# Kernel tuning notes

Hardware: AMD Instinct MI355X
Metric: run time of the kernel (lower is better)

The kernel has to match this reference:

```python
import jax, jax.numpy as jnp
import numpy as np

B, FR, D = 32, 300, 2048
E, G, K = 2, 8, 64
FEAT = E * D // G          # 512
VLAD = K * FEAT            # 32768
H, R = 2048, 8
NC = 3862
BN_EPS = 1e-5
L2_EPS = 1e-12


def _bn(x, g, b, m, v):
    # eval-mode BatchNorm1d with running stats
    return (x - m) * jax.lax.rsqrt(v + BN_EPS) * g + b


def _l2n(x, axis):
    # torch F.normalize: x / max(||x||, eps)
    n = jnp.sqrt(jnp.sum(x * x, axis=axis, keepdims=True))
    return x / jnp.maximum(n, L2_EPS)


def setup_inputs() -> dict:
    key = jax.random.key(0)
    ks = jax.random.split(key, 10)
    rn = lambda k, s: jax.random.normal(k, s, jnp.float32) * 0.02
    return {
        "x": jax.random.normal(ks[0], (B, FR, D), jnp.float32),
        "fc1_w": rn(ks[1], (E * D, D)), "fc1_b": jnp.zeros((E * D,), jnp.float32),
        "fc2_w": rn(ks[2], (G, E * D)), "fc2_b": jnp.zeros((G,), jnp.float32),
        "c1": jax.random.uniform(ks[3], (E * D, G * K), jnp.float32),
        "c2": jax.random.uniform(ks[4], (1, FEAT, K), jnp.float32),
        "bn1_g": jnp.ones((G * K,), jnp.float32), "bn1_b": jnp.zeros((G * K,), jnp.float32),
        "bn1_m": jnp.zeros((G * K,), jnp.float32), "bn1_v": jnp.ones((G * K,), jnp.float32),
        "bn2_g": jnp.ones((VLAD,), jnp.float32), "bn2_b": jnp.zeros((VLAD,), jnp.float32),
        "bn2_m": jnp.zeros((VLAD,), jnp.float32), "bn2_v": jnp.ones((VLAD,), jnp.float32),
        "cgf_w": rn(ks[5], (H, VLAD)), "cgf_b": jnp.zeros((H,), jnp.float32),
        "cgbn_g": jnp.ones((H,), jnp.float32), "cgbn_b": jnp.zeros((H,), jnp.float32),
        "cgbn_m": jnp.zeros((H,), jnp.float32), "cgbn_v": jnp.ones((H,), jnp.float32),
        "g1_w": rn(ks[6], (H // R, H)), "g1_b": jnp.zeros((H // R,), jnp.float32),
        "gbn_g": jnp.ones((H // R,), jnp.float32), "gbn_b": jnp.zeros((H // R,), jnp.float32),
        "gbn_m": jnp.zeros((H // R,), jnp.float32), "gbn_v": jnp.ones((H // R,), jnp.float32),
        "g2_w": rn(ks[7], (H, H // R)), "g2_b": jnp.zeros((H,), jnp.float32),
        "fc3_w": rn(ks[8], (NC, H)), "fc3_b": jnp.zeros((NC,), jnp.float32),
    }


def _forward(x, fc1_w, fc1_b, fc2_w, fc2_b, c1, c2,
             bn1_g, bn1_b, bn1_m, bn1_v, bn2_g, bn2_b, bn2_m, bn2_v,
             cgf_w, cgf_b, cgbn_g, cgbn_b, cgbn_m, cgbn_v,
             g1_w, g1_b, gbn_g, gbn_b, gbn_m, gbn_v, g2_w, g2_b, fc3_w, fc3_b):
    b, fr, d = x.shape
    xn = _l2n(x, 2)                                      # per-frame L2 normalize
    h = xn @ fc1_w.T + fc1_b                             # [B,FR,E*D]
    att = jax.nn.sigmoid(h @ fc2_w.T + fc2_b)            # [B,FR,G]
    att = att.reshape(b, fr * G, 1)
    act = jnp.einsum('bfd,dc->bfc', h, c1)               # [B,FR,G*K]
    act = _bn(act, bn1_g, bn1_b, bn1_m, bn1_v)
    act = act.reshape(b, fr * G, K)
    act = jax.nn.softmax(act, axis=-1) * att             # soft-assign * attention
    a = act.sum(axis=1, keepdims=True) * c2              # [B,FEAT,K] via broadcast
    res = h.reshape(b, fr * G, FEAT)
    vlad = jnp.einsum('bnk,bnf->bfk', act, res) - a      # [B,FEAT,K]
    vlad = _l2n(vlad, 1).reshape(b, VLAD)                # intra-norm, flatten feat-major
    vlad = _bn(vlad, bn2_g, bn2_b, bn2_m, bn2_v)
    # SE context gating (dropout identity in reference)
    y = _bn(vlad @ cgf_w.T + cgf_b, cgbn_g, cgbn_b, cgbn_m, cgbn_v)   # [B,H]
    gate = jax.nn.sigmoid(
        jax.nn.relu(_bn(y @ g1_w.T + g1_b, gbn_g, gbn_b, gbn_m, gbn_v)) @ g2_w.T + g2_b)
    return (y * gate) @ fc3_w.T + fc3_b                  # [B,NC]


def reference(x, fc1_w, fc1_b, fc2_w, fc2_b, c1, c2,
              bn1_g, bn1_b, bn1_m, bn1_v, bn2_g, bn2_b, bn2_m, bn2_v,
              cgf_w, cgf_b, cgbn_g, cgbn_b, cgbn_m, cgbn_v,
              g1_w, g1_b, gbn_g, gbn_b, gbn_m, gbn_v, g2_w, g2_b, fc3_w, fc3_b):
    return _forward(x, fc1_w, fc1_b, fc2_w, fc2_b, c1, c2,
                    bn1_g, bn1_b, bn1_m, bn1_v, bn2_g, bn2_b, bn2_m, bn2_v,
                    cgf_w, cgf_b, cgbn_g, cgbn_b, cgbn_m, cgbn_v,
                    g1_w, g1_b, gbn_g, gbn_b, gbn_m, gbn_v, g2_w, g2_b, fc3_w, fc3_b)
```

## Files before the change

### kernel.cpp

```cpp
#include <hip/hip_runtime.h>

typedef unsigned short u16;
typedef unsigned int u32;
using f32x4 = __attribute__((ext_vector_type(4))) float;
using s16x8 = __attribute__((ext_vector_type(8))) short;
using u16x4 = __attribute__((ext_vector_type(4))) u16;

#define DEV __device__ __forceinline__

DEV float bf2f(u16 u) { union { u32 i; float f; } v; v.i = ((u32)u) << 16; return v.f; }
DEV u16 f2bf(float f) {
  union { float ff; u32 uu; } v; v.ff = f;
  u32 r = (v.uu + 0x7fffu + ((v.uu >> 16) & 1u)) >> 16;
  return (u16)r;
}

DEV void gl_lds16(const void* g, void* l) {
  __builtin_amdgcn_global_load_lds(
      (const __attribute__((address_space(1))) u32*)g,
      (__attribute__((address_space(3))) u32*)l, 16, 0, 0);
}

DEV void BAR() { __builtin_amdgcn_s_barrier(); }
DEV void VM6() { asm volatile("s_waitcnt vmcnt(6)" ::: "memory"); }
DEV void VM0() { asm volatile("s_waitcnt vmcnt(0)" ::: "memory"); }
DEV void PRIO1() { __builtin_amdgcn_s_setprio(1); }
DEV void PRIO0() { __builtin_amdgcn_s_setprio(0); }
#define LGKM0S() do { asm volatile("s_waitcnt lgkmcnt(0)" ::: "memory"); \
                      __builtin_amdgcn_sched_barrier(0); } while (0)

#define DSR(d, a, OFF) asm volatile("ds_read_b128 %0, %1 offset:" #OFF \
                                    : "=&v"(d) : "v"(a))
#define READ12(A_, B_, aa, bb) do {                                            \
  unsigned a_ = (aa), b_ = (bb);                                               \
  DSR(A_[0], a_, 0);     DSR(A_[1], a_, 2048);                                 \
  DSR(A_[2], a_, 4096);  DSR(A_[3], a_, 6144);                                 \
  DSR(A_[4], a_, 8192);  DSR(A_[5], a_, 10240);                                \
  DSR(A_[6], a_, 12288); DSR(A_[7], a_, 14336);                                \
  DSR(B_[0], b_, 0);     DSR(B_[1], b_, 2048);                                 \
  DSR(B_[2], b_, 4096);  DSR(B_[3], b_, 6144);                                 \
} while (0)

#define MFMA32(A_, B_) do {                                                    \
  _Pragma("unroll")                                                            \
  for (int i_ = 0; i_ < 8; i_++) {                                             \
    acc[i_][0] = __builtin_amdgcn_mfma_f32_16x16x32_bf16(A_[i_], B_[0], acc[i_][0], 0, 0, 0); \
    acc[i_][1] = __builtin_amdgcn_mfma_f32_16x16x32_bf16(A_[i_], B_[1], acc[i_][1], 0, 0, 0); \
    acc[i_][2] = __builtin_amdgcn_mfma_f32_16x16x32_bf16(A_[i_], B_[2], acc[i_][2], 0, 0, 0); \
    acc[i_][3] = __builtin_amdgcn_mfma_f32_16x16x32_bf16(A_[i_], B_[3], acc[i_][3], 0, 0, 0); \
  }                                                                            \
} while (0)

__global__ __launch_bounds__(256) void k_l2norm(const float* __restrict__ x, u16* __restrict__ xn) {
  int r = blockIdx.x, t = threadIdx.x;
  const float* xr = x + (size_t)r * 2048;
  float v[8], s = 0.f;
#pragma unroll
  for (int i = 0; i < 8; i++) { v[i] = xr[t + i*256]; s += v[i]*v[i]; }
#pragma unroll
  for (int off = 32; off > 0; off >>= 1) s += __shfl_xor(s, off, 64);
  __shared__ float red[4];
  if ((t & 63) == 0) red[t >> 6] = s;
  __syncthreads();
  float inv = 1.f / fmaxf(sqrtf(red[0]+red[1]+red[2]+red[3]), 1e-12f);
  u16* xo = xn + (size_t)r * 2048;
#pragma unroll
  for (int i = 0; i < 8; i++) xo[t + i*256] = f2bf(v[i]*inv);
}

__global__ void k_cvt(const float* __restrict__ in, u16* __restrict__ out, int n4) {
  int i = blockIdx.x*256 + threadIdx.x, st = gridDim.x*256;
  for (; i < n4; i += st) {
    f32x4 v = ((const f32x4*)in)[i];
    u16x4 o;
    o[0] = f2bf(v[0]); o[1] = f2bf(v[1]); o[2] = f2bf(v[2]); o[3] = f2bf(v[3]);
    ((u16x4*)out)[i] = o;
  }
}

__global__ __launch_bounds__(256) void k_transpose(const float* __restrict__ c1, u16* __restrict__ c1t) {
  __shared__ float tile[32][33];
  int k0 = blockIdx.x*32, n0 = blockIdx.y*32;
  int tx = threadIdx.x & 31, ty = threadIdx.x >> 5;
  for (int i = ty; i < 32; i += 8) tile[i][tx] = c1[(size_t)(k0+i)*512 + n0 + tx];
  __syncthreads();
  for (int i = ty; i < 32; i += 8) c1t[(size_t)(n0+i)*4096 + k0 + tx] = f2bf(tile[tx][i]);
}

template<bool WF32, bool WBF16>
__global__ __launch_bounds__(256) void k_gemm(
    const u16* __restrict__ A, const u16* __restrict__ Bt, const float* __restrict__ bias,
    float* __restrict__ Cf, u16* __restrict__ Cb, int N, int K, int Nlim,
    int MT, int NT, int swz) {
  __shared__ u16 As[128*32];
  __shared__ u16 Bs[128*32];
  int bid = blockIdx.x, mt, nt;
  if (swz) {
    int mg = (MT + 7) >> 3;
    int gid = bid >> 5, gl = bid & 31;
    mt = (gid % mg)*8 + (gl & 7);
    nt = (gid / mg)*4 + (gl >> 3);
    if (mt >= MT) return;
  } else { mt = bid % MT; nt = bid / MT; }
  int t = threadIdx.x, wv = t >> 6;
  int quad = (t & 63) >> 4, lr = t & 15;
  size_t m0 = (size_t)mt * 128, n0 = (size_t)nt * 128;
  int wm = wv & 1, wn = wv >> 1;
  int srow = t >> 2;
  int scol = (((t & 3) ^ ((t >> 3) & 3)) * 8);
  const u16* gA = A + (m0 + srow)*(size_t)K + scol;
  const u16* gB = Bt + (n0 + srow)*(size_t)K + scol;
  u16* lA = &As[wv*512];
  u16* lB = &Bs[wv*512];
  int xq = (quad ^ ((lr >> 1) & 3)) * 8;
  f32x4 acc[4][4];
#pragma unroll
  for (int i = 0; i < 4; i++)
#pragma unroll
    for (int j = 0; j < 4; j++) acc[i][j] = (f32x4){0.f,0.f,0.f,0.f};
  for (int k0 = 0; k0 < K; k0 += 32) {
    gl_lds16(gA + k0, lA);
    gl_lds16(gA + (size_t)64*K + k0, lA + 2048);
    gl_lds16(gB + k0, lB);
    gl_lds16(gB + (size_t)64*K + k0, lB + 2048);
    __syncthreads();
    s16x8 af[4], bfr[4];
#pragma unroll
    for (int i = 0; i < 4; i++) {
      af[i]  = *(const s16x8*)&As[(wm*64 + i*16 + lr)*32 + xq];
      bfr[i] = *(const s16x8*)&Bs[(wn*64 + i*16 + lr)*32 + xq];
    }
#pragma unroll
    for (int i = 0; i < 4; i++)
#pragma unroll
      for (int j = 0; j < 4; j++)
        acc[i][j] = __builtin_amdgcn_mfma_f32_16x16x32_bf16(af[i], bfr[j], acc[i][j], 0, 0, 0);
    __syncthreads();
  }
#pragma unroll
  for (int j = 0; j < 4; j++) {
    size_t nn = n0 + wn*64 + j*16 + lr;
    if ((int)nn >= Nlim) continue;
    float bj = bias ? bias[nn] : 0.f;
#pragma unroll
    for (int i = 0; i < 4; i++) {
      size_t mr = m0 + wm*64 + i*16 + quad*4;
#pragma unroll
      for (int r = 0; r < 4; r++) {
        float v = acc[i][j][r] + bj;
        if (WF32)  Cf[(mr + r)*N + nn] = v;
        if (WBF16) Cb[(mr + r)*N + nn] = f2bf(v);
      }
    }
  }
}

template<bool WF32, bool WBF16>
__global__ __launch_bounds__(512, 2) void k_gemm256(
    const u16* __restrict__ A, const u16* __restrict__ Bt, const float* __restrict__ bias,
    float* __restrict__ Cf, u16* __restrict__ Cb,
    int M, int N, int K, int Nlim, int MT, int NT, int swz) {
  constexpr int TILE = 256*64;
  __shared__ u16 lds[4*TILE];
  int bid = blockIdx.x, mt, nt;
  if (swz == 2) {
    int x = bid & 7, w2 = bid >> 3;
    mt = (x & 1)*19 + w2 % 19;
    nt = (x >> 1)*4 + w2 / 19;
  } else if (swz == 1) {
    int c = (MT*NT) >> 3; int b2 = (bid & 7)*c + (bid >> 3);
    mt = b2 % MT; nt = b2 / MT;
  } else { mt = bid % MT; nt = bid / MT; }
  int t = threadIdx.x, wv = t >> 6, lane = t & 63;
  int quad = lane >> 4, lr = lane & 15;
  int wm = wv >> 2, wn = wv & 3;
  size_t m0 = (size_t)mt * 256, n0 = (size_t)nt * 256;
  int srow = wv*8 + (lane >> 3);
  int schunk = ((lane & 7) ^ (lane >> 3)) * 8;
  const u16* gA = A  + (size_t)(m0 + srow)*K + schunk;
  const u16* gB = Bt + (size_t)(n0 + srow)*K + schunk;
  size_t row64 = (size_t)64 * K;
  int lofs = wv*512;
  unsigned ldsB = (unsigned)(size_t)lds;
  unsigned pc = (unsigned)((quad ^ (lr & 7)) << 4);
  unsigned aCur = ldsB + (unsigned)((wm*128 + lr)*128) + pc;
  unsigned bCur = ldsB + 32768u + (unsigned)((wn*64 + lr)*128) + pc;
  f32x4 acc[8][4];
#pragma unroll
  for (int i = 0; i < 8; i++)
#pragma unroll
    for (int j = 0; j < 4; j++) acc[i][j] = (f32x4){0.f,0.f,0.f,0.f};

  int T = K >> 6;
  u16* A0 = lds;            u16* B0 = lds + TILE;
  u16* A1 = lds + 2*TILE;   u16* B1 = lds + 3*TILE;
#pragma unroll
  for (int q = 0; q < 4; q++) gl_lds16(gA + q*row64, A0 + q*4096 + lofs);
#pragma unroll
  for (int q = 0; q < 4; q++) gl_lds16(gB + q*row64, B0 + q*4096 + lofs);
#pragma unroll
  for (int q = 0; q < 4; q++) gl_lds16(gA + 64 + q*row64, A1 + q*4096 + lofs);
  gl_lds16(gB + 64,          B1 + lofs);
  gl_lds16(gB + 64 + row64,  B1 + 4096 + lofs);
  VM6();
  BAR();

  s16x8 fa[8], fb[4];
  for (int tt = 0; tt < T; ++tt) {
    READ12(fa, fb, aCur, bCur);
    if (tt + 1 < T) {
      const u16* gB1 = gB + (size_t)(tt + 1)*64;
      u16* Bq = lds + (((tt + 1) & 1)*2 + 1)*TILE;
      gl_lds16(gB1 + 2*row64, Bq + 2*4096 + lofs);
      gl_lds16(gB1 + 3*row64, Bq + 3*4096 + lofs);
    }
    LGKM0S();
    PRIO1(); MFMA32(fa, fb); PRIO0();
    BAR();
    READ12(fa, fb, aCur ^ 64u, bCur ^ 64u);
    LGKM0S();
    PRIO1(); MFMA32(fa, fb); PRIO0();
    BAR();
    if (tt + 2 < T) {
      const u16* gA2 = gA + (size_t)(tt + 2)*64;
      const u16* gB2 = gB + (size_t)(tt + 2)*64;
      u16* Ap = lds + ((tt & 1)*2)*TILE;
      u16* Bp = Ap + TILE;
#pragma unroll
      for (int q = 0; q < 4; q++) gl_lds16(gA2 + q*row64, Ap + q*4096 + lofs);
      gl_lds16(gB2,         Bp + lofs);
      gl_lds16(gB2 + row64, Bp + 4096 + lofs);
      VM6();
    } else if (tt + 1 < T) {
      VM0();
    }
    if (tt + 1 < T) BAR();
    aCur ^= 0x10000u; bCur ^= 0x10000u;
  }

  float bj[4];
#pragma unroll
  for (int j = 0; j < 4; j++) {
    int nn = (int)n0 + wn*64 + j*16 + lr;
    bj[j] = (bias && nn < Nlim) ? bias[nn] : 0.f;
  }
#pragma unroll
  for (int i = 0; i < 8; i++) {
    int mrb = (int)m0 + wm*128 + i*16 + quad*4;
#pragma unroll
    for (int r = 0; r < 4; r++) {
      int mr = mrb + r;
      if (mr >= M) continue;
#pragma unroll
      for (int j = 0; j < 4; j++) {
        int nn = (int)n0 + wn*64 + j*16 + lr;
        if (nn >= Nlim) continue;
        float v = acc[i][j][r] + bj[j];
        if (WF32)  Cf[(size_t)mr*N + nn] = v;
        if (WBF16) Cb[(size_t)mr*N + nn] = f2bf(v);
      }
    }
  }
}

__global__ __launch_bounds__(256) void k_hbt(const u16* __restrict__ hb, u16* __restrict__ hbT) {
  __shared__ u16 tile[64*33];
  int nt = blockIdx.x, ft = blockIdx.y, b = blockIdx.z, t = threadIdx.x;
  int n0 = nt*32, f0 = ft*64;
  int rrel = t >> 6, g = (t >> 3) & 7, fi = (t & 7)*8;
  const u16* src = hb + ((size_t)(b*300 + (n0 >> 3) + rrel))*4096 + g*512 + f0 + fi;
  u16 v[8];
  *(u16x4*)v = *(const u16x4*)src;
  *(u16x4*)(v+4) = *(const u16x4*)(src+4);
  int nl = rrel*8 + g;
#pragma unroll
  for (int e = 0; e < 8; e++) tile[(fi+e)*33 + nl] = v[e];
  __syncthreads();
  int f = t >> 2, nc = (t & 3)*8;
  u16 o[8];
#pragma unroll
  for (int e = 0; e < 8; e++) o[e] = tile[f*33 + nc + e];
  u16* dst = hbT + ((size_t)b*512 + f0 + f)*2400 + n0 + nc;
  *(u16x4*)dst = *(u16x4*)o;
  *(u16x4*)(dst+4) = *(u16x4*)(o+4);
}

__global__ __launch_bounds__(512) void k_softmax(const float* __restrict__ act_ext,
    const float* __restrict__ fc2_b,
    const float* __restrict__ g, const float* __restrict__ b,
    const float* __restrict__ mu, const float* __restrict__ var, u16* __restrict__ actT) {
  int m = blockIdx.x, t = threadIdx.x;
  int bb = m / 300, fr = m - bb*300;
  int gi = t >> 6, k = t & 63, c = t;
  float v = act_ext[(size_t)m*640 + c];
  v = (v - mu[c]) * rsqrtf(var[c] + 1e-5f) * g[c] + b[c];
  float mx = v;
#pragma unroll
  for (int off = 32; off > 0; off >>= 1) mx = fmaxf(mx, __shfl_xor(mx, off, 64));
  float e = __expf(v - mx);
  float s = e;
#pragma unroll
  for (int off = 32; off > 0; off >>= 1) s += __shfl_xor(s, off, 64);
  float attl = act_ext[(size_t)m*640 + 512 + gi] + fc2_b[gi];
  float attv = 1.f / (1.f + __expf(-attl));
  float r = (e / s) * attv;
  __shared__ u16 st[64*9];
  st[k*9 + gi] = f2bf(r);
  __syncthreads();
  if (t < 64) {
    u16 o[8];
#pragma unroll
    for (int e2 = 0; e2 < 8; e2++) o[e2] = st[t*9 + e2];
    u16* dst = actT + ((size_t)bb*64 + t)*2400 + fr*8;
    *(u16x4*)dst = *(u16x4*)o;
    *(u16x4*)(dst+4) = *(u16x4*)(o+4);
  }
}

__global__ __launch_bounds__(256) void k_asum(const u16* __restrict__ actT, float* __restrict__ a_sum) {
  int b = blockIdx.x, t = threadIdx.x;
  int k = t >> 2, q = t & 3;
  const u16* p = actT + ((size_t)b*64 + k)*2400 + q*600;
  float acc = 0.f;
  for (int j = 0; j < 600; j += 8) {
    u16x4 a0 = *(const u16x4*)(p + j);
    u16x4 a1 = *(const u16x4*)(p + j + 4);
    acc += bf2f(a0[0])+bf2f(a0[1])+bf2f(a0[2])+bf2f(a0[3])
         + bf2f(a1[0])+bf2f(a1[1])+bf2f(a1[2])+bf2f(a1[3]);
  }
  __shared__ float red[256];
  red[t] = acc;
  __syncthreads();
  if (t < 64) a_sum[b*64 + t] = red[t*4] + red[t*4+1] + red[t*4+2] + red[t*4+3];
}

__global__ __launch_bounds__(256) void k_vlad(const u16* __restrict__ hbT, const u16* __restrict__ actT,
                                              float* __restrict__ P2) {
  __shared__ u16 As[128*32];
  __shared__ u16 Bs[64*32];
  int t = threadIdx.x, wv = t >> 6;
  int quad = (t & 63) >> 4, lr = t & 15;
  int ft = blockIdx.x, b = blockIdx.y, ns = blockIdx.z;
  int wm = wv & 1, wn = wv >> 1;
  int srow = t >> 2;
  int scol = (((t & 3) ^ ((t >> 3) & 3)) * 8);
  int xq = (quad ^ ((lr >> 1) & 3)) * 8;
  const u16* gA = hbT + ((size_t)b*512 + ft*128 + srow)*2400 + ns*480 + scol;
  const u16* gB = actT + ((size_t)b*64 + srow)*2400 + ns*480 + scol;
  u16* lA = &As[wv*512];
  u16* lB = &Bs[wv*512];
  f32x4 acc[4][2];
#pragma unroll
  for (int i = 0; i < 4; i++)
#pragma unroll
    for (int j = 0; j < 2; j++) acc[i][j] = (f32x4){0.f,0.f,0.f,0.f};
  for (int k0 = 0; k0 < 480; k0 += 32) {
    gl_lds16(gA + k0, lA);
    gl_lds16(gA + (size_t)64*2400 + k0, lA + 2048);
    gl_lds16(gB + k0, lB);
    __syncthreads();
    s16x8 af[4], bfr[2];
#pragma unroll
    for (int i = 0; i < 4; i++)
      af[i] = *(const s16x8*)&As[(wm*64 + i*16 + lr)*32 + xq];
#pragma unroll
    for (int j = 0; j < 2; j++)
      bfr[j] = *(const s16x8*)&Bs[(wn*32 + j*16 + lr)*32 + xq];
#pragma unroll
    for (int i = 0; i < 4; i++)
#pragma unroll
      for (int j = 0; j < 2; j++)
        acc[i][j] = __builtin_amdgcn_mfma_f32_16x16x32_bf16(af[i], bfr[j], acc[i][j], 0, 0, 0);
    __syncthreads();
  }
  size_t base = ((size_t)ns*32 + b)*512*64;
#pragma unroll
  for (int j = 0; j < 2; j++) {
    int kc = wn*32 + j*16 + lr;
#pragma unroll
    for (int i = 0; i < 4; i++) {
      int f = ft*128 + wm*64 + i*16 + quad*4;
#pragma unroll
      for (int r = 0; r < 4; r++)
        P2[base + (size_t)(f + r)*64 + kc] = acc[i][j][r];
    }
  }
}

__global__ __launch_bounds__(256) void k_norm2(const float* __restrict__ P2, const float* __restrict__ a_sum,
    const float* __restrict__ c2, const float* __restrict__ g, const float* __restrict__ b,
    const float* __restrict__ mu, const float* __restrict__ var, float* __restrict__ out) {
  int k = blockIdx.x, bb = blockIdx.y, t = threadIdx.x;
  float as = a_sum[bb*64 + k];
  int f0 = t, f1 = t + 256;
  const size_t PS = (size_t)32*512*64;
  size_t base = (size_t)bb*512*64;
  float x0 = 0.f, x1 = 0.f;
#pragma unroll
  for (int ns = 0; ns < 5; ns++) {
    x0 += P2[ns*PS + base + (size_t)f0*64 + k];
    x1 += P2[ns*PS + base + (size_t)f1*64 + k];
  }
  x0 -= as * c2[f0*64 + k];
  x1 -= as * c2[f1*64 + k];
  float s = x0*x0 + x1*x1;
#pragma unroll
  for (int off = 32; off > 0; off >>= 1) s += __shfl_xor(s, off, 64);
  __shared__ float red[4];
  if ((t & 63) == 0) red[t >> 6] = s;
  __syncthreads();
  float inv = 1.f / fmaxf(sqrtf(red[0]+red[1]+red[2]+red[3]), 1e-12f);
  int c0 = f0*64 + k, c1 = f1*64 + k;
  out[(size_t)bb*32768 + c0] = (x0*inv - mu[c0]) * rsqrtf(var[c0]+1e-5f) * g[c0] + b[c0];
  out[(size_t)bb*32768 + c1] = (x1*inv - mu[c1]) * rsqrtf(var[c1]+1e-5f) * g[c1] + b[c1];
}

__global__ __launch_bounds__(256) void k_skgemm(
    const float* __restrict__ A, const float* __restrict__ W,
    float* __restrict__ P, int N, int K, int KC, int Npad) {
  constexpr int LDB = 72;
  __shared__ u16 Bs[128*LDB];
  __shared__ u16 As[32*LDB];
  int t = threadIdx.x;
  int wv = t >> 6, quad = (t & 63) >> 4, lr = t & 15;
  int n0 = blockIdx.x * 128;
  size_t kc0 = (size_t)blockIdx.y * KC;
  f32x4 acc[2][2];
#pragma unroll
  for (int i = 0; i < 2; i++)
#pragma unroll
    for (int j = 0; j < 2; j++) acc[i][j] = (f32x4){0.f,0.f,0.f,0.f};
  int wl[8]; size_t wg[8];
#pragma unroll
  for (int i = 0; i < 8; i++) {
    int slot = i*256 + t;
    int r = slot >> 4, q = slot & 15;
    int row = n0 + r; if (row >= N) row = N - 1;
    wl[i] = r*LDB + q*4;
    wg[i] = (size_t)row*K + kc0 + q*4;
  }
  int al[2]; size_t ag[2];
#pragma unroll
  for (int i = 0; i < 2; i++) {
    int slot = i*256 + t;
    int r = slot >> 4, q = slot & 15;
    al[i] = r*LDB + q*4;
    ag[i] = (size_t)r*K + kc0 + q*4;
  }
  int nst = KC >> 6;
  f32x4 wv4[8], av4[2];
#pragma unroll
  for (int i = 0; i < 8; i++) wv4[i] = *(const f32x4*)(W + wg[i]);
#pragma unroll
  for (int i = 0; i < 2; i++) av4[i] = *(const f32x4*)(A + ag[i]);
  for (int s = 0; s < nst; s++) {
    if (s) __syncthreads();
#pragma unroll
    for (int i = 0; i < 8; i++) {
      u16x4 o;
      o[0] = f2bf(wv4[i][0]); o[1] = f2bf(wv4[i][1]);
      o[2] = f2bf(wv4[i][2]); o[3] = f2bf(wv4[i][3]);
      *(u16x4*)&Bs[wl[i]] = o;
    }
#pragma unroll
    for (int i = 0; i < 2; i++) {
      u16x4 o;
      o[0] = f2bf(av4[i][0]); o[1] = f2bf(av4[i][1]);
      o[2] = f2bf(av4[i][2]); o[3] = f2bf(av4[i][3]);
      *(u16x4*)&As[al[i]] = o;
    }
    __syncthreads();
    if (s + 1 < nst) {
      int off = (s + 1) * 64;
#pragma unroll
      for (int i = 0; i < 8; i++) wv4[i] = *(const f32x4*)(W + wg[i] + off);
#pragma unroll
      for (int i = 0; i < 2; i++) av4[i] = *(const f32x4*)(A + ag[i] + off);
    }
#pragma unroll
    for (int ks = 0; ks < 2; ks++) {
      s16x8 af[2];
#pragma unroll
      for (int i = 0; i < 2; i++)
        af[i] = *(const s16x8*)&As[(i*16 + lr)*LDB + ks*32 + quad*8];
#pragma unroll
      for (int j = 0; j < 2; j++) {
        s16x8 bf = *(const s16x8*)&Bs[(wv*32 + j*16 + lr)*LDB + ks*32 + quad*8];
#pragma unroll
        for (int i = 0; i < 2; i++)
          acc[i][j] = __builtin_amdgcn_mfma_f32_16x16x32_bf16(af[i], bf, acc[i][j], 0, 0, 0);
      }
    }
  }
#pragma unroll
  for (int i = 0; i < 2; i++)
#pragma unroll
    for (int j = 0; j < 2; j++) {
      int n = n0 + wv*32 + j*16 + lr;
#pragma unroll
      for (int r = 0; r < 4; r++) {
        int m = i*16 + quad*4 + r;
        P[((size_t)blockIdx.y*32 + m)*Npad + n] = acc[i][j][r];
      }
    }
}

template<int EPI>
__global__ __launch_bounds__(256) void k_skred(const float* __restrict__ P, int KSPLIT, int N, int Npad,
    const float* __restrict__ bias, const float* __restrict__ bg, const float* __restrict__ bb,
    const float* __restrict__ bm, const float* __restrict__ bv, float* __restrict__ C) {
  int idx = blockIdx.x*256 + threadIdx.x;
  if (idx >= 32*N) return;
  int m = idx / N, n = idx - m*N;
  float s = 0.f;
  for (int k = 0; k < KSPLIT; k++) s += P[((size_t)k*32 + m)*Npad + n];
  float v = s + (bias ? bias[n] : 0.f);
  if (EPI == 1 || EPI == 2) {
    v = (v - bm[n]) * rsqrtf(bv[n] + 1e-5f) * bg[n] + bb[n];
    if (EPI == 2) v = fmaxf(v, 0.f);
  } else if (EPI == 3) {
    v = 1.f / (1.f + __expf(-v));
  }
  C[idx] = v;
}

__global__ void k_mul(const float* __restrict__ a, const float* __restrict__ b, float* __restrict__ o, int n) {
  int i = blockIdx.x*256 + threadIdx.x;
  if (i < n) o[i] = a[i]*b[i];
}

extern "C" void kernel_launch(void* const* d_in, const int* in_sizes, int n_in,
                              void* d_out, int out_size, void* d_ws, size_t ws_size,
                              hipStream_t stream) {
  (void)in_sizes; (void)n_in; (void)out_size; (void)ws_size;
  const float* x      = (const float*)d_in[0];
  const float* fc1_w  = (const float*)d_in[1];
  const float* fc1_b  = (const float*)d_in[2];
  const float* fc2_w  = (const float*)d_in[3];
  const float* fc2_b  = (const float*)d_in[4];
  const float* c1     = (const float*)d_in[5];
  const float* c2     = (const float*)d_in[6];
  const float* bn1_g  = (const float*)d_in[7];
  const float* bn1_b  = (const float*)d_in[8];
  const float* bn1_m  = (const float*)d_in[9];
  const float* bn1_v  = (const float*)d_in[10];
  const float* bn2_g  = (const float*)d_in[11];
  const float* bn2_b  = (const float*)d_in[12];
  const float* bn2_m  = (const float*)d_in[13];
  const float* bn2_v  = (const float*)d_in[14];
  const float* cgf_w  = (const float*)d_in[15];
  const float* cgf_b  = (const float*)d_in[16];
  const float* cgbn_g = (const float*)d_in[17];
  const float* cgbn_b = (const float*)d_in[18];
  const float* cgbn_m = (const float*)d_in[19];
  const float* cgbn_v = (const float*)d_in[20];
  const float* g1_w   = (const float*)d_in[21];
  const float* g1_b   = (const float*)d_in[22];
  const float* gbn_g  = (const float*)d_in[23];
  const float* gbn_b  = (const float*)d_in[24];
  const float* gbn_m  = (const float*)d_in[25];
  const float* gbn_v  = (const float*)d_in[26];
  const float* g2_w   = (const float*)d_in[27];
  const float* g2_b   = (const float*)d_in[28];
  const float* fc3_w  = (const float*)d_in[29];
  const float* fc3_b  = (const float*)d_in[30];

  char* w = (char*)d_ws;
  u16*   xn    = (u16*)  (w + 0);
  u16*   w1b   = (u16*)  (w + 39321600);
  u16*   hbT   = (u16*)  (w + 0);
  u16*   hb    = (u16*)  (w + 78643200);
  u16*   c1ext = (u16*)  (w + 157286400);
  float* actx  = (float*)(w + 162529280);
  u16*   actT  = (u16*)  (w + 187105280);
  float* P2    = (float*)(w + 196935680);
  float* P     = (float*)(w + 196935680);
  float* a_sum = (float*)(w + 217907200);
  float* vladn = (float*)(w + 217915392);
  float* y     = (float*)(w + 222109696);
  float* z     = (float*)(w + 222371840);
  float* gate  = (float*)(w + 222404608);
  float* yg    = (float*)(w + 222666752);

  k_l2norm<<<9600, 256, 0, stream>>>(x, xn);
  k_cvt<<<2048, 256, 0, stream>>>(fc1_w, w1b, (4096*2048)/4);
  k_transpose<<<dim3(128, 16), 256, 0, stream>>>(c1, c1ext);
  k_cvt<<<32, 256, 0, stream>>>(fc2_w, c1ext + (size_t)512*4096, (8*4096)/4);
  k_gemm256<false, true><<<608, 512, 0, stream>>>(xn, w1b, fc1_b, nullptr, hb,
                                                  9600, 4096, 2048, 4096, 38, 16, 2);
  k_hbt<<<dim3(75, 8, 32), 256, 0, stream>>>(hb, hbT);
  k_gemm<true, false><<<375, 256, 0, stream>>>(hb, c1ext, nullptr, actx, nullptr, 640, 4096, 520, 75, 5, 0);
  k_softmax<<<9600, 512, 0, stream>>>(actx, fc2_b, bn1_g, bn1_b, bn1_m, bn1_v, actT);
  k_asum<<<32, 256, 0, stream>>>(actT, a_sum);
  k_vlad<<<dim3(4, 32, 5), 256, 0, stream>>>(hbT, actT, P2);
  k_norm2<<<dim3(64, 32), 256, 0, stream>>>(P2, a_sum, c2, bn2_g, bn2_b, bn2_m, bn2_v, vladn);

  k_skgemm<<<dim3(16, 64), 256, 0, stream>>>(vladn, cgf_w, P, 2048, 32768, 512, 2048);
  k_skred<1><<<256, 256, 0, stream>>>(P, 64, 2048, 2048, cgf_b, cgbn_g, cgbn_b, cgbn_m, cgbn_v, y);
  k_skgemm<<<dim3(2, 32), 256, 0, stream>>>(y, g1_w, P, 256, 2048, 64, 256);
  k_skred<2><<<32, 256, 0, stream>>>(P, 32, 256, 256, g1_b, gbn_g, gbn_b, gbn_m, gbn_v, z);
  k_skgemm<<<dim3(16, 4), 256, 0, stream>>>(z, g2_w, P, 2048, 256, 64, 2048);
  k_skred<3><<<256, 256, 0, stream>>>(P, 4, 2048, 2048, g2_b, nullptr, nullptr, nullptr, nullptr, gate);
  k_mul<<<256, 256, 0, stream>>>(y, gate, yg, 65536);
  k_skgemm<<<dim3(31, 16), 256, 0, stream>>>(yg, fc3_w, P, 3862, 2048, 128, 3968);
  k_skred<0><<<483, 256, 0, stream>>>(P, 16, 3862, 3968, fc3_b, nullptr, nullptr, nullptr, nullptr, (float*)d_out);
}
```

Baseline: 1.003 ms.

## Software-pipeline LDS fragment reads with MFMA in GEMM main loop

The GEMM inner loop now reads LDS fragments in quarter-sized groups into double-buffered register sets. Partial lgkmcnt waits let each group of 16 MFMAs run while the next ds_reads are in flight, replacing the old read-all-then-wait-all pattern. One mid-iteration barrier is removed and the next tile's first fragments are prefetched across the loop boundary. This costs more VGPRs for the extra fragment buffers, which may lower occupancy, and depends on the lgkmcnt counts exactly matching the issue order of the reads.

New measurement: 992.0 us. About the same (-1.1%).

```diff
diff --git a/kernel.cpp b/kernel.cpp
--- a/kernel.cpp
+++ b/kernel.cpp
@@ -21,35 +21,29 @@
       (__attribute__((address_space(3))) u32*)l, 16, 0, 0);
 }
 
-DEV void BAR() { __builtin_amdgcn_s_barrier(); }
+DEV void BAR() { __builtin_amdgcn_s_barrier(); __builtin_amdgcn_sched_barrier(0); }
 DEV void VM6() { asm volatile("s_waitcnt vmcnt(6)" ::: "memory"); }
 DEV void VM0() { asm volatile("s_waitcnt vmcnt(0)" ::: "memory"); }
 DEV void PRIO1() { __builtin_amdgcn_s_setprio(1); }
 DEV void PRIO0() { __builtin_amdgcn_s_setprio(0); }
-#define LGKM0S() do { asm volatile("s_waitcnt lgkmcnt(0)" ::: "memory"); \
-                      __builtin_amdgcn_sched_barrier(0); } while (0)
+#define SBAR0() __builtin_amdgcn_sched_barrier(0)
+#define LGKM(N_) do { asm volatile("s_waitcnt lgkmcnt(" #N_ ")" ::: "memory"); SBAR0(); } while (0)
 
 #define DSR(d, a, OFF) asm volatile("ds_read_b128 %0, %1 offset:" #OFF \
                                     : "=&v"(d) : "v"(a))
-#define READ12(A_, B_, aa, bb) do {                                            \
-  unsigned a_ = (aa), b_ = (bb);                                               \
-  DSR(A_[0], a_, 0);     DSR(A_[1], a_, 2048);                                 \
-  DSR(A_[2], a_, 4096);  DSR(A_[3], a_, 6144);                                 \
-  DSR(A_[4], a_, 8192);  DSR(A_[5], a_, 10240);                                \
-  DSR(A_[6], a_, 12288); DSR(A_[7], a_, 14336);                                \
-  DSR(B_[0], b_, 0);     DSR(B_[1], b_, 2048);                                 \
-  DSR(B_[2], b_, 4096);  DSR(B_[3], b_, 6144);                                 \
-} while (0)
-
-#define MFMA32(A_, B_) do {                                                    \
+#define DSR4(D_, a_) do { unsigned aa_ = (a_);                                 \
+  DSR(D_[0], aa_, 0);    DSR(D_[1], aa_, 2048);                                \
+  DSR(D_[2], aa_, 4096); DSR(D_[3], aa_, 6144); } while (0)
+
+#define MF16(FA_, FB_, R_) do { PRIO1();                                       \
   _Pragma("unroll")                                                            \
-  for (int i_ = 0; i_ < 8; i_++) {                                             \
-    acc[i_][0] = __builtin_amdgcn_mfma_f32_16x16x32_bf16(A_[i_], B_[0], acc[i_][0], 0, 0, 0); \
-    acc[i_][1] = __builtin_amdgcn_mfma_f32_16x16x32_bf16(A_[i_], B_[1], acc[i_][1], 0, 0, 0); \
-    acc[i_][2] = __builtin_amdgcn_mfma_f32_16x16x32_bf16(A_[i_], B_[2], acc[i_][2], 0, 0, 0); \
-    acc[i_][3] = __builtin_amdgcn_mfma_f32_16x16x32_bf16(A_[i_], B_[3], acc[i_][3], 0, 0, 0); \
+  for (int i_ = 0; i_ < 4; i_++) {                                             \
+    acc[(R_)+i_][0] = __builtin_amdgcn_mfma_f32_16x16x32_bf16(FA_[i_], FB_[0], acc[(R_)+i_][0], 0, 0, 0); \
+    acc[(R_)+i_][1] = __builtin_amdgcn_mfma_f32_16x16x32_bf16(FA_[i_], FB_[1], acc[(R_)+i_][1], 0, 0, 0); \
+    acc[(R_)+i_][2] = __builtin_amdgcn_mfma_f32_16x16x32_bf16(FA_[i_], FB_[2], acc[(R_)+i_][2], 0, 0, 0); \
+    acc[(R_)+i_][3] = __builtin_amdgcn_mfma_f32_16x16x32_bf16(FA_[i_], FB_[3], acc[(R_)+i_][3], 0, 0, 0); \
   }                                                                            \
-} while (0)
+  PRIO0(); } while (0)
 
 __global__ __launch_bounds__(256) void k_l2norm(const float* __restrict__ x, u16* __restrict__ xn) {
   int r = blockIdx.x, t = threadIdx.x;
@@ -205,21 +199,31 @@
   VM6();
   BAR();
 
-  s16x8 fa[8], fb[4];
+  s16x8 FAA[4], FAB[4], FBA[4], FBB[4];
+  DSR4(FBA, bCur);
+  DSR4(FAA, aCur);
+  SBAR0();
+
   for (int tt = 0; tt < T; ++tt) {
-    READ12(fa, fb, aCur, bCur);
+    DSR4(FAB, aCur + 8192u);
+    SBAR0();
+    LGKM(4);
+    MF16(FAA, FBA, 0);
+    DSR4(FBB, bCur ^ 64u);
+    DSR4(FAA, aCur ^ 64u);
     if (tt + 1 < T) {
       const u16* gB1 = gB + (size_t)(tt + 1)*64;
       u16* Bq = lds + (((tt + 1) & 1)*2 + 1)*TILE;
       gl_lds16(gB1 + 2*row64, Bq + 2*4096 + lofs);
       gl_lds16(gB1 + 3*row64, Bq + 3*4096 + lofs);
     }
-    LGKM0S();
-    PRIO1(); MFMA32(fa, fb); PRIO0();
-    BAR();
-    READ12(fa, fb, aCur ^ 64u, bCur ^ 64u);
-    LGKM0S();
-    PRIO1(); MFMA32(fa, fb); PRIO0();
+    SBAR0();
+    LGKM(8);
+    MF16(FAB, FBA, 4);
+    DSR4(FAB, (aCur + 8192u) ^ 64u);
+    SBAR0();
+    LGKM(4);
+    MF16(FAA, FBB, 0);
     BAR();
     if (tt + 2 < T) {
       const u16* gA2 = gA + (size_t)(tt + 2)*64;
@@ -235,6 +239,15 @@
       VM0();
     }
     if (tt + 1 < T) BAR();
+    if (tt + 1 < T) {
+      DSR4(FBA, bCur ^ 0x10000u);
+      DSR4(FAA, aCur ^ 0x10000u);
+      SBAR0();
+      LGKM(8);
+    } else {
+      LGKM(0);
+    }
+    MF16(FAB, FBB, 4);
     aCur ^= 0x10000u; bCur ^= 0x10000u;
   }
 
```
